# Kernel tuning notes

Measured on AMD Instinct MI355X. Metric: run time of the kernel, lower is better.

Reference implementation:

```python
import jax, jax.numpy as jnp
import numpy as np

B = 32; N = 512; SEQ_LEN = 8
L = 0.05; T_REF = 5.0; V_TH = 20.0; V_RES = 0.0
SQL = float(np.sqrt(L))
BN_EPS = 1e-5

# ---- Dawson-style lookup tables for the LIF moment activation (built once, float64) ----
_XG = np.linspace(-10.0, 4.0, 7001)
_DX = _XG[1] - _XG[0]

def _cumtrapz(y):
    return np.concatenate([[0.0], np.cumsum(0.5 * (y[1:] + y[:-1]) * _DX)])

_phi = np.exp(-_XG ** 2)
_I = np.exp(-100.0) / 20.0 + _cumtrapz(_phi)          # int_{-inf}^x e^{-t^2} dt (asymptotic tail at -10)
_g = np.exp(_XG ** 2) * _I                             # 1st Dawson-like function g(x)
_G = _cumtrapz(_g)                                     # int g dx (rel. to -10)
_h = np.exp(_XG ** 2) * _cumtrapz(_phi * _g ** 2)      # 2nd Dawson-like function h(x)
_H = _cumtrapz(_h)                                     # int h dx

XG = jnp.asarray(_XG, jnp.float32)
GT = jnp.asarray(_g, jnp.float32)
GI = jnp.asarray(_G, jnp.float32)
HI = jnp.asarray(_H, jnp.float32)

def _interp(x, tab):
    return jnp.interp(x, XG, tab)

def moment_activate(u, s, rho):
    # Mnn_Activate_Mean / Std / Corr: LIF moment activation
    s = jnp.maximum(s, 1e-6)
    ub = jnp.clip((V_TH * L - u) / (s * SQL), -10.0, 4.0)
    lb = jnp.clip((V_RES * L - u) / (s * SQL), -10.0, 4.0)
    dG = _interp(ub, GI) - _interp(lb, GI)
    ua = 1.0 / (T_REF + (2.0 / L) * dG)                               # mean firing rate
    dH = jnp.maximum(_interp(ub, HI) - _interp(lb, HI), 0.0)
    sa = jnp.sqrt((8.0 / L ** 2) * dH * ua ** 3)                      # firing std
    dg = _interp(ub, GT) - _interp(lb, GT)
    chi = ua ** 2 * (2.0 / L) * dg / (SQL * jnp.maximum(sa, 1e-9))    # linear response coeff
    eye = jnp.eye(rho.shape[-1], dtype=rho.dtype)
    rho_out = chi[:, :, None] * chi[:, None, :] * rho                 # [B,N,N]
    rho_out = rho_out * (1.0 - eye) + eye                             # unit diagonal
    return ua, sa, rho_out

def linear_corr(W, b, u, s, rho):
    # Mnn_Linear_Corr: mean via affine map, covariance via W C W^T
    u_out = u @ W.T + b
    Cin = rho * s[:, :, None] * s[:, None, :]                         # [B,N,N] covariance
    C = jnp.einsum('bik,lk->bil', jnp.einsum('ij,bjk->bik', W, Cin), W)
    var = jnp.clip(jnp.diagonal(C, axis1=1, axis2=2), 0.0, None)
    s_out = jnp.sqrt(var)
    denom = s_out[:, :, None] * s_out[:, None, :]
    rho_out = jnp.where(denom > 1e-12, C / jnp.maximum(denom, 1e-12), 0.0)
    return u_out, s_out, rho_out

def mexi_hat(n, k=0.3):
    dx = 2.0 * np.pi / n
    x = np.arange(0.0, 2.0 * np.pi, dx)[:n]
    y = np.exp(2.0 * (np.cos(x) - 1.0)) * np.cos(2.0 * x)
    j = np.arange(n)
    idx = (j[None, :] - j[:, None]) % n                               # w[i,:] = y.roll(i)
    return y[idx].astype(np.float32)

def setup_inputs() -> dict:
    ks = jax.random.split(jax.random.key(0), 10)
    u = jax.random.normal(ks[0], (B, N), jnp.float32)
    s = jax.random.uniform(ks[1], (B, N), jnp.float32, 0.1, 1.0)
    A = jax.random.normal(ks[2], (B, N, N), jnp.float32) / np.sqrt(N)
    sym = 0.5 * (A + jnp.swapaxes(A, 1, 2))
    eye = jnp.eye(N, dtype=jnp.float32)
    rho = jnp.clip(sym, -0.5, 0.5) * (1.0 - eye) + eye                # valid-ish corr matrix
    u_ext = jax.random.normal(ks[3], (B, N), jnp.float32)
    s_ext = jax.random.uniform(ks[4], (B, N), jnp.float32, 0.1, 1.0)
    W = 0.02 * jax.random.normal(ks[5], (N, N), jnp.float32) + 0.1 * jnp.asarray(mexi_hat(N))
    b = 0.02 * jax.random.normal(ks[6], (N,), jnp.float32)
    W_ext = 0.02 * jax.random.normal(ks[7], (N, N), jnp.float32)
    b_ext = 0.02 * jax.random.normal(ks[8], (N,), jnp.float32)
    w_mean = 2.5 * jnp.ones((N,), jnp.float32)
    b_mean = 2.5 * jnp.ones((N,), jnp.float32)
    w_mean_ext = 2.5 * jnp.ones((N,), jnp.float32)
    b_mean_ext = 2.5 * jnp.ones((N,), jnp.float32)
    return {'u': u, 's': s, 'rho': rho, 'u_ext': u_ext, 's_ext': s_ext,
            'W': W, 'b': b, 'W_ext': W_ext, 'b_ext': b_ext,
            'w_mean': w_mean, 'b_mean': b_mean,
            'w_mean_ext': w_mean_ext, 'b_mean_ext': b_mean_ext,
            'seq_len': SEQ_LEN}

def reference(u, s, rho, u_ext, s_ext, W, b, W_ext, b_ext,
              w_mean, b_mean, w_mean_ext, b_mean_ext, seq_len):
    # external pathway (Mnn_Linear_without_Corr + BN), computed once
    u_e = u_ext @ W_ext.T + b_ext
    s_e = jnp.sqrt((s_ext ** 2) @ (W_ext ** 2).T)
    mean_e = jnp.mean(u_e, axis=0); var_e = jnp.var(u_e, axis=0)
    f_e = w_mean_ext / jnp.sqrt(var_e + BN_EPS)
    s_e = s_e * jnp.abs(f_e)                                          # Mnn_Std_Bn1d (uses pre-BN stats)
    u_e = (u_e - mean_e) * f_e + b_mean_ext

    def step(carry, _):
        u, s, rho = carry
        u, s, rho = linear_corr(W, b, u, s, rho)
        mean = jnp.mean(u, axis=0); var = jnp.var(u, axis=0)
        f = w_mean / jnp.sqrt(var + BN_EPS)
        s = s * jnp.abs(f)
        u = (u - mean) * f + b_mean
        u = u + u_e
        s = jnp.sqrt(s * s + s_e * s_e)
        return moment_activate(u, s, rho), None

    (u, s, rho), _ = jax.lax.scan(step, (u, s, rho), None, length=seq_len)
    return u, s, rho
```

## Files before the change

### kernel.cpp

```cpp
#include <hip/hip_runtime.h>
#include <math.h>


#define BB 32
#define NN 512
#define SEQ 8
#define TG 7001

typedef float f32x4 __attribute__((ext_vector_type(4)));
typedef short s16x8 __attribute__((ext_vector_type(8)));

#define GL16(g, l) __builtin_amdgcn_global_load_lds( \
    (const __attribute__((address_space(1))) void*)(g), \
    (__attribute__((address_space(3))) void*)(l), 16, 0, 0)

__device__ __forceinline__ unsigned short bf16_rne(float v) {
    unsigned u = __float_as_uint(v);
    u += 0x7FFFu + ((u >> 16) & 1u);
    return (unsigned short)(u >> 16);
}
__device__ __forceinline__ float bf16_f(unsigned short h) {
    return __uint_as_float(((unsigned)h) << 16);
}
__device__ __forceinline__ void split2(float v, unsigned short& h, unsigned short& l) {
    unsigned short hh = bf16_rne(v);
    h = hh;
    l = bf16_rne(v - bf16_f(hh));
}

__device__ __forceinline__ float interp_tab(const float* __restrict__ tab, float x) {
    float t = (x + 10.0f) * 500.0f;
    t = fminf(fmaxf(t, 0.0f), 7000.0f);
    int i0 = (int)t;
    if (i0 > 6999) i0 = 6999;
    float fr = t - (float)i0;
    float a = tab[i0];
    float b = tab[i0 + 1];
    return a + fr * (b - a);
}

__device__ double blk_exscan(double part, double* wsum) {
    int t = threadIdx.x, lane = t & 63, wid = t >> 6;
    double run = part;
    #pragma unroll
    for (int off = 1; off < 64; off <<= 1) {
        double nv = __shfl_up(run, off);
        if (lane >= off) run += nv;
    }
    if (lane == 63) wsum[wid] = run;
    __syncthreads();
    if (t < 16) {
        double v = wsum[t];
        #pragma unroll
        for (int off = 1; off < 16; off <<= 1) {
            double nv = __shfl_up(v, off);
            if (lane >= off) v += nv;
        }
        wsum[t] = v;
    }
    __syncthreads();
    double base = (wid > 0) ? wsum[wid - 1] : 0.0;
    double ex = base + run - part;
    __syncthreads();
    return ex;
}

__global__ __launch_bounds__(1024)
void k_tables(double* __restrict__ expP, double* __restrict__ expM,
              double* __restrict__ gd, double* __restrict__ Ed,
              float* __restrict__ GT, float* __restrict__ GI, float* __restrict__ HI) {
    __shared__ double wsum[16];
    const int t = threadIdx.x;
    const double dx = 14.0 / 7000.0;
    int k0 = t * 7, k1 = k0 + 7;
    if (k1 > TG) k1 = TG;
    if (k0 > TG) k0 = TG;

    for (int k = k0; k < k1; ++k) {
        double x = -10.0 + dx * k;
        expP[k] = exp(x * x);
        expM[k] = exp(-x * x);
    }
    __syncthreads();

    {
        double part = 0.0;
        for (int k = (k0 < 1 ? 1 : k0); k < k1; ++k)
            part += 0.5 * (expM[k - 1] + expM[k]) * dx;
        double run = blk_exscan(part, wsum) + exp(-100.0) / 20.0;
        for (int k = k0; k < k1; ++k) {
            if (k >= 1) run += 0.5 * (expM[k - 1] + expM[k]) * dx;
            double g = expP[k] * run;
            gd[k] = g;
            GT[k] = (float)g;
        }
    }
    __syncthreads();
    {
        double part = 0.0;
        for (int k = (k0 < 1 ? 1 : k0); k < k1; ++k)
            part += 0.5 * (gd[k - 1] + gd[k]) * dx;
        double run = blk_exscan(part, wsum);
        for (int k = k0; k < k1; ++k) {
            if (k >= 1) run += 0.5 * (gd[k - 1] + gd[k]) * dx;
            GI[k] = (float)run;
        }
    }
    __syncthreads();
    {
        double part = 0.0;
        for (int k = (k0 < 1 ? 1 : k0); k < k1; ++k) {
            double ya = expM[k - 1] * gd[k - 1] * gd[k - 1];
            double yb = expM[k] * gd[k] * gd[k];
            part += 0.5 * (ya + yb) * dx;
        }
        double run = blk_exscan(part, wsum);
        for (int k = k0; k < k1; ++k) {
            if (k >= 1) {
                double ya = expM[k - 1] * gd[k - 1] * gd[k - 1];
                double yb = expM[k] * gd[k] * gd[k];
                run += 0.5 * (ya + yb) * dx;
            }
            Ed[k] = run;
        }
    }
    __syncthreads();
    {
        double part = 0.0;
        for (int k = (k0 < 1 ? 1 : k0); k < k1; ++k)
            part += 0.5 * (expP[k - 1] * Ed[k - 1] + expP[k] * Ed[k]) * dx;
        double run = blk_exscan(part, wsum);
        for (int k = k0; k < k1; ++k) {
            if (k >= 1) run += 0.5 * (expP[k - 1] * Ed[k - 1] + expP[k] * Ed[k]) * dx;
            HI[k] = (float)run;
        }
    }
}

__global__ void k_splitW(const float* __restrict__ W,
                         unsigned short* __restrict__ Wh, unsigned short* __restrict__ Wl) {
    int idx = blockIdx.x * 256 + threadIdx.x;
    unsigned short h, l;
    split2(W[idx], h, l);
    Wh[idx] = h; Wl[idx] = l;
}

__global__ void k_splitQ(const float* __restrict__ rho, const float* __restrict__ s,
                         unsigned short* __restrict__ Qh, unsigned short* __restrict__ Ql) {
    size_t idx = (size_t)blockIdx.x * 256 + threadIdx.x;
    int b = (int)(idx >> 18);
    int i = (int)((idx >> 9) & 511);
    int j = (int)(idx & 511);
    float v = rho[idx] * s[b * NN + i] * s[b * NN + j];
    unsigned short h, l;
    split2(v, h, l);
    Qh[idx] = h; Ql[idx] = l;
}

template <int MODE>
__global__ __launch_bounds__(256)
void gemm_mfma(const unsigned short* __restrict__ Ah, const unsigned short* __restrict__ Al,
               long aStride,
               const unsigned short* __restrict__ Bh, const unsigned short* __restrict__ Bl,
               long bStride,
               unsigned short* __restrict__ Oh, unsigned short* __restrict__ Ol,
               float* __restrict__ Of,
               const float* __restrict__ s_lin, const float* __restrict__ chi,
               const float* __restrict__ s_next) {
    __shared__ unsigned short As0[4096], As1[4096], Bs0[4096], Bs1[4096];
    const int b = blockIdx.z;
    const int i0 = blockIdx.y * 128, j0 = blockIdx.x * 128;
    const int tid = threadIdx.x;
    const int w = tid >> 6, lane = tid & 63;
    const int wm = w >> 1, wn = w & 1;

    const unsigned short* Ab_h = Ah + (size_t)b * aStride;
    const unsigned short* Ab_l = Al + (size_t)b * aStride;
    const unsigned short* Bb_h = Bh + (size_t)b * bStride;
    const unsigned short* Bb_l = Bl + (size_t)b * bStride;

    const size_t gA0 = ((size_t)(i0 + (w * 2 + 0) * 16 + (lane >> 2)) << 9) + ((lane & 3) << 3);
    const size_t gA1 = ((size_t)(i0 + (w * 2 + 1) * 16 + (lane >> 2)) << 9) + ((lane & 3) << 3);
    const size_t gB0 = ((size_t)(j0 + (w * 2 + 0) * 16 + (lane >> 2)) << 9) + ((lane & 3) << 3);
    const size_t gB1 = ((size_t)(j0 + (w * 2 + 1) * 16 + (lane >> 2)) << 9) + ((lane & 3) << 3);
    const int lds0 = (w * 2 + 0) * 512;
    const int lds1 = (w * 2 + 1) * 512;

    f32x4 acc[4][4];
    #pragma unroll
    for (int m = 0; m < 4; ++m)
        #pragma unroll
        for (int n = 0; n < 4; ++n) acc[m][n] = (f32x4){0.f, 0.f, 0.f, 0.f};

    const int kg = lane >> 4;
    int aoff[4], boff[4];
    #pragma unroll
    for (int t = 0; t < 4; ++t) {
        aoff[t] = (wm * 64 + t * 16 + (lane & 15)) * 32 + kg * 8;
        boff[t] = (wn * 64 + t * 16 + (lane & 15)) * 32 + kg * 8;
    }

    for (int k0 = 0; k0 < NN; k0 += 32) {
        GL16(Ab_h + gA0 + k0, As0 + lds0);
        GL16(Ab_h + gA1 + k0, As0 + lds1);
        GL16(Ab_l + gA0 + k0, As1 + lds0);
        GL16(Ab_l + gA1 + k0, As1 + lds1);
        GL16(Bb_h + gB0 + k0, Bs0 + lds0);
        GL16(Bb_h + gB1 + k0, Bs0 + lds1);
        GL16(Bb_l + gB0 + k0, Bs1 + lds0);
        GL16(Bb_l + gB1 + k0, Bs1 + lds1);
        __syncthreads();
        s16x8 ah[4], al[4], bh[4], bl[4];
        #pragma unroll
        for (int t = 0; t < 4; ++t) {
            ah[t] = *reinterpret_cast<const s16x8*>(&As0[aoff[t]]);
            al[t] = *reinterpret_cast<const s16x8*>(&As1[aoff[t]]);
            bh[t] = *reinterpret_cast<const s16x8*>(&Bs0[boff[t]]);
            bl[t] = *reinterpret_cast<const s16x8*>(&Bs1[boff[t]]);
        }
        #pragma unroll
        for (int m = 0; m < 4; ++m)
            #pragma unroll
            for (int n = 0; n < 4; ++n) {
                acc[m][n] = __builtin_amdgcn_mfma_f32_16x16x32_bf16(ah[m], bh[n], acc[m][n], 0, 0, 0);
                acc[m][n] = __builtin_amdgcn_mfma_f32_16x16x32_bf16(ah[m], bl[n], acc[m][n], 0, 0, 0);
                acc[m][n] = __builtin_amdgcn_mfma_f32_16x16x32_bf16(al[m], bh[n], acc[m][n], 0, 0, 0);
            }
        __syncthreads();
    }

    const size_t bofs = (size_t)b * NN * NN;
    const int rb = i0 + wm * 64 + (lane >> 4) * 4;
    const int cb = j0 + wn * 64 + (lane & 15);

    if (MODE == 0) {
        #pragma unroll
        for (int m = 0; m < 4; ++m)
            #pragma unroll
            for (int n = 0; n < 4; ++n) {
                int col = cb + n * 16;
                #pragma unroll
                for (int r = 0; r < 4; ++r) {
                    int row = rb + m * 16 + r;
                    size_t idx = bofs + ((size_t)row << 9) + col;
                    unsigned short h, l;
                    split2(acc[m][n][r], h, l);
                    Oh[idx] = h; Ol[idx] = l;
                }
            }
    } else {
        const float* sl = s_lin + b * NN;
        const float* ch = chi + b * NN;
        float sj[4], cj[4], qj[4];
        #pragma unroll
        for (int n = 0; n < 4; ++n) {
            int col = cb + n * 16;
            sj[n] = sl[col];
            cj[n] = ch[col];
            if (MODE == 1) qj[n] = s_next[b * NN + col];
        }
        #pragma unroll
        for (int m = 0; m < 4; ++m)
            #pragma unroll
            for (int r = 0; r < 4; ++r) {
                int row = rb + m * 16 + r;
                float si = sl[row], ci = ch[row];
                float qi = (MODE == 1) ? s_next[b * NN + row] : 0.f;
                #pragma unroll
                for (int n = 0; n < 4; ++n) {
                    int col = cb + n * 16;
                    float denom = si * sj[n];
                    float rv = (denom > 1e-12f) ? (acc[m][n][r] / fmaxf(denom, 1e-12f)) : 0.0f;
                    rv *= ci * cj[n];
                    if (row == col) rv = 1.0f;
                    size_t idx = bofs + ((size_t)row << 9) + col;
                    if (MODE == 1) {
                        unsigned short h, l;
                        split2(rv * qi * qj[n], h, l);
                        Oh[idx] = h; Ol[idx] = l;
                    } else {
                        Of[idx] = rv;
                    }
                }
            }
    }
}

__global__ void k_ext_dots(const float* __restrict__ Wx, const float* __restrict__ bx,
                           const float* __restrict__ ux, const float* __restrict__ sx,
                           float* __restrict__ u_e, float* __restrict__ s_e2) {
    int gw = (blockIdx.x << 2) + (threadIdx.x >> 6);
    int lane = threadIdx.x & 63;
    int b = gw >> 9, i = gw & 511;
    const float* wr = Wx + (size_t)i * NN;
    const float* ub = ux + b * NN;
    const float* sb = sx + b * NN;
    float au = 0.0f, as2 = 0.0f;
    for (int j = lane; j < NN; j += 64) {
        float w = wr[j];
        float s = sb[j];
        au = fmaf(w, ub[j], au);
        as2 = fmaf(w * w, s * s, as2);
    }
    #pragma unroll
    for (int off = 32; off; off >>= 1) {
        au += __shfl_down(au, off);
        as2 += __shfl_down(as2, off);
    }
    if (lane == 0) {
        u_e[b * NN + i] = au + bx[i];
        s_e2[b * NN + i] = as2;
    }
}

__global__ void k_ext_stats(float* __restrict__ u_e, float* __restrict__ s_e2,
                            const float* __restrict__ wmx, const float* __restrict__ bmx) {
    int i = blockIdx.x * blockDim.x + threadIdx.x;
    if (i >= NN) return;
    float m = 0.0f;
    for (int b = 0; b < BB; ++b) m += u_e[b * NN + i];
    m *= (1.0f / BB);
    float v = 0.0f;
    for (int b = 0; b < BB; ++b) {
        float d = u_e[b * NN + i] - m;
        v = fmaf(d, d, v);
    }
    v *= (1.0f / BB);
    float f = wmx[i] / sqrtf(v + 1e-5f);
    float bm = bmx[i];
    for (int b = 0; b < BB; ++b) {
        u_e[b * NN + i] = (u_e[b * NN + i] - m) * f + bm;
        s_e2[b * NN + i] *= f * f;
    }
}

__global__ void k_dots(const float* __restrict__ W, const float* __restrict__ bvec,
                       const float* __restrict__ u,
                       const unsigned short* __restrict__ T1h,
                       const unsigned short* __restrict__ T1l,
                       float* __restrict__ u_lin, float* __restrict__ s_lin) {
    int gw = (blockIdx.x << 2) + (threadIdx.x >> 6);
    int lane = threadIdx.x & 63;
    int b = gw >> 9, i = gw & 511;
    const float* wr = W + (size_t)i * NN;
    const float* ub = u + b * NN;
    const unsigned short* th = T1h + ((size_t)b * NN + i) * NN;
    const unsigned short* tl = T1l + ((size_t)b * NN + i) * NN;
    float au = 0.0f, ad = 0.0f;
    for (int j = lane; j < NN; j += 64) {
        float wv = wr[j];
        au = fmaf(wv, ub[j], au);
        float tv = bf16_f(th[j]) + bf16_f(tl[j]);
        ad = fmaf(wv, tv, ad);
    }
    #pragma unroll
    for (int off = 32; off; off >>= 1) {
        au += __shfl_down(au, off);
        ad += __shfl_down(ad, off);
    }
    if (lane == 0) {
        u_lin[b * NN + i] = au + bvec[i];
        s_lin[b * NN + i] = sqrtf(fmaxf(ad, 0.0f));
    }
}

__global__ void k_stats(const float* __restrict__ u_lin, const float* __restrict__ wm,
                        float* __restrict__ bn_mean, float* __restrict__ bn_f) {
    int i = blockIdx.x * blockDim.x + threadIdx.x;
    if (i >= NN) return;
    float m = 0.0f;
    for (int b = 0; b < BB; ++b) m += u_lin[b * NN + i];
    m *= (1.0f / BB);
    float v = 0.0f;
    for (int b = 0; b < BB; ++b) {
        float d = u_lin[b * NN + i] - m;
        v = fmaf(d, d, v);
    }
    v *= (1.0f / BB);
    bn_mean[i] = m;
    bn_f[i] = wm[i] / sqrtf(v + 1e-5f);
}

__global__ void k_act(const float* __restrict__ u_lin, const float* __restrict__ s_lin,
                      const float* __restrict__ bn_mean, const float* __restrict__ bn_f,
                      const float* __restrict__ b_mean,
                      const float* __restrict__ u_e, const float* __restrict__ s_e2,
                      const float* __restrict__ GT, const float* __restrict__ GI,
                      const float* __restrict__ HI,
                      float* __restrict__ u_out, float* __restrict__ s_out,
                      float* __restrict__ chi) {
    int idx = blockIdx.x * blockDim.x + threadIdx.x;
    int i = idx & 511;
    const float SQL = 0.22360679774997896f;
    float f = bn_f[i];
    float un = (u_lin[idx] - bn_mean[i]) * f + b_mean[i] + u_e[idx];
    float sl = s_lin[idx];
    float sn = sqrtf(sl * sl * f * f + s_e2[idx]);
    float ss = fmaxf(sn, 1e-6f);
    float inv = 1.0f / (ss * SQL);
    float ubx = fminf(fmaxf((1.0f - un) * inv, -10.0f), 4.0f);
    float lbx = fminf(fmaxf((0.0f - un) * inv, -10.0f), 4.0f);
    float dG = interp_tab(GI, ubx) - interp_tab(GI, lbx);
    float ua = 1.0f / (5.0f + 40.0f * dG);
    float dH = fmaxf(interp_tab(HI, ubx) - interp_tab(HI, lbx), 0.0f);
    float sa = sqrtf(3200.0f * dH * ua * ua * ua);
    float dg = interp_tab(GT, ubx) - interp_tab(GT, lbx);
    float ch = ua * ua * 40.0f * dg / (SQL * fmaxf(sa, 1e-9f));
    u_out[idx] = ua;
    s_out[idx] = sa;
    chi[idx] = ch;
}

extern "C" void kernel_launch(void* const* d_in, const int* in_sizes, int n_in,
                              void* d_out, int out_size, void* d_ws, size_t ws_size,
                              hipStream_t stream) {
    (void)in_sizes; (void)n_in; (void)out_size; (void)ws_size;
    const float* u_in       = (const float*)d_in[0];
    const float* s_in       = (const float*)d_in[1];
    const float* rho_in     = (const float*)d_in[2];
    const float* u_ext      = (const float*)d_in[3];
    const float* s_ext      = (const float*)d_in[4];
    const float* W          = (const float*)d_in[5];
    const float* bvec       = (const float*)d_in[6];
    const float* W_ext      = (const float*)d_in[7];
    const float* b_ext      = (const float*)d_in[8];
    const float* w_mean     = (const float*)d_in[9];
    const float* b_mean     = (const float*)d_in[10];
    const float* w_mean_ext = (const float*)d_in[11];
    const float* b_mean_ext = (const float*)d_in[12];

    float* out_u   = (float*)d_out;
    float* out_s   = out_u + BB * NN;
    float* out_rho = out_s + BB * NN;
    unsigned short* Qh = (unsigned short*)out_rho;
    unsigned short* Ql = Qh + (size_t)BB * NN * NN;

    char* base = (char*)d_ws;
    size_t off = 0;
    auto alloc = [&](size_t bytes) -> char* {
        char* p = base + off;
        off += (bytes + 255) & ~(size_t)255;
        return p;
    };
    unsigned short* T1h = (unsigned short*)alloc((size_t)BB * NN * NN * 2);
    unsigned short* T1l = (unsigned short*)alloc((size_t)BB * NN * NN * 2);
    unsigned short* Wh  = (unsigned short*)alloc((size_t)NN * NN * 2);
    unsigned short* Wl  = (unsigned short*)alloc((size_t)NN * NN * 2);
    double* expP = (double*)alloc(TG * 8);
    double* expM = (double*)alloc(TG * 8);
    double* gd   = (double*)alloc(TG * 8);
    double* Ed   = (double*)alloc(TG * 8);
    float* GTt   = (float*)alloc(TG * 4);
    float* GIt   = (float*)alloc(TG * 4);
    float* HIt   = (float*)alloc(TG * 4);
    float* u_e   = (float*)alloc(BB * NN * 4);
    float* s_e2  = (float*)alloc(BB * NN * 4);
    float* uA    = (float*)alloc(BB * NN * 4);
    float* uB2   = (float*)alloc(BB * NN * 4);
    float* sA    = (float*)alloc(BB * NN * 4);
    float* sB2   = (float*)alloc(BB * NN * 4);
    float* u_lin = (float*)alloc(BB * NN * 4);
    float* s_lin = (float*)alloc(BB * NN * 4);
    float* chi_  = (float*)alloc(BB * NN * 4);
    float* bn_m  = (float*)alloc(NN * 4);
    float* bn_f  = (float*)alloc(NN * 4);

    k_tables<<<1, 1024, 0, stream>>>(expP, expM, gd, Ed, GTt, GIt, HIt);
    k_splitW<<<NN * NN / 256, 256, 0, stream>>>(W, Wh, Wl);
    k_splitQ<<<BB * NN * NN / 256, 256, 0, stream>>>(rho_in, s_in, Qh, Ql);
    k_ext_dots<<<BB * NN / 4, 256, 0, stream>>>(W_ext, b_ext, u_ext, s_ext, u_e, s_e2);
    k_ext_stats<<<2, 256, 0, stream>>>(u_e, s_e2, w_mean_ext, b_mean_ext);

    const float* cu = u_in;
    dim3 gg(NN / 128, NN / 128, BB);

    for (int t = 0; t < SEQ; ++t) {
        gemm_mfma<0><<<gg, 256, 0, stream>>>(
            Wh, Wl, 0L, Qh, Ql, (long)NN * NN, T1h, T1l, nullptr, nullptr, nullptr, nullptr);
        k_dots<<<BB * NN / 4, 256, 0, stream>>>(W, bvec, cu, T1h, T1l, u_lin, s_lin);
        k_stats<<<2, 256, 0, stream>>>(u_lin, w_mean, bn_m, bn_f);
        float* nu = (t == SEQ - 1) ? out_u : ((t & 1) ? uA : uB2);
        float* ns = (t == SEQ - 1) ? out_s : ((t & 1) ? sA : sB2);
        k_act<<<BB * NN / 256, 256, 0, stream>>>(
            u_lin, s_lin, bn_m, bn_f, b_mean, u_e, s_e2, GTt, GIt, HIt, nu, ns, chi_);
        if (t < SEQ - 1) {
            gemm_mfma<1><<<gg, 256, 0, stream>>>(
                T1h, T1l, (long)NN * NN, Wh, Wl, 0L, Qh, Ql, nullptr, s_lin, chi_, ns);
        } else {
            gemm_mfma<2><<<gg, 256, 0, stream>>>(
                T1h, T1l, (long)NN * NN, Wh, Wl, 0L, nullptr, nullptr, out_rho, s_lin, chi_, nullptr);
        }
        cu = nu;
    }
}
```

Before: 833.9 us.

## Fuse diagonal variance into GEMM epilogue, swizzle tiles, parallelize table build

The first GEMM epilogue now computes each row's diagonal variance dot product against W and accumulates it with atomics. This removes the pass in k_dots that reread the full T1 intermediate. BN statistics and the activation are merged into one small kernel, and the GEMM grid is flattened with a swizzle that groups tiles sharing operands. The table construction moves exp into a parallel kernel and keeps the scan intermediates in shared memory. The trade-offs are atomics, a 2-block activation kernel that serializes over the batch, and extra W reads in the epilogue.

Result: slower. 924.0 us (+10.8%).

```diff
diff --git a/kernel.cpp b/kernel.cpp
--- a/kernel.cpp
+++ b/kernel.cpp
@@ -39,6 +39,14 @@
     return a + fr * (b - a);
 }
 
+__global__ void k_exp(double* __restrict__ expP, double* __restrict__ expM) {
+    int k = blockIdx.x * 256 + threadIdx.x;
+    if (k >= TG) return;
+    double x = -10.0 + (14.0 / 7000.0) * k;
+    expP[k] = exp(x * x);
+    expM[k] = exp(-x * x);
+}
+
 __device__ double blk_exscan(double part, double* wsum) {
     int t = threadIdx.x, lane = t & 63, wid = t >> 6;
     double run = part;
@@ -66,72 +74,76 @@
 }
 
 __global__ __launch_bounds__(1024)
-void k_tables(double* __restrict__ expP, double* __restrict__ expM,
-              double* __restrict__ gd, double* __restrict__ Ed,
-              float* __restrict__ GT, float* __restrict__ GI, float* __restrict__ HI) {
+void k_scan(const double* __restrict__ expP, const double* __restrict__ expM,
+            float* __restrict__ GT, float* __restrict__ GI, float* __restrict__ HI) {
+    __shared__ double ys[7008];
     __shared__ double wsum[16];
     const int t = threadIdx.x;
     const double dx = 14.0 / 7000.0;
     int k0 = t * 7, k1 = k0 + 7;
     if (k1 > TG) k1 = TG;
     if (k0 > TG) k0 = TG;
-
-    for (int k = k0; k < k1; ++k) {
-        double x = -10.0 + dx * k;
-        expP[k] = exp(x * x);
-        expM[k] = exp(-x * x);
-    }
+    int kls = (k0 < 1) ? 1 : k0;
+
+    for (int k = k0; k < k1; ++k) ys[k] = expM[k];
     __syncthreads();
 
+    double tmp[7];
     {
         double part = 0.0;
-        for (int k = (k0 < 1 ? 1 : k0); k < k1; ++k)
-            part += 0.5 * (expM[k - 1] + expM[k]) * dx;
+        for (int k = kls; k < k1; ++k) part += 0.5 * (ys[k - 1] + ys[k]) * dx;
         double run = blk_exscan(part, wsum) + exp(-100.0) / 20.0;
+        int c = 0;
         for (int k = k0; k < k1; ++k) {
-            if (k >= 1) run += 0.5 * (expM[k - 1] + expM[k]) * dx;
-            double g = expP[k] * run;
-            gd[k] = g;
-            GT[k] = (float)g;
-        }
-    }
-    __syncthreads();
+            if (k >= 1) run += 0.5 * (ys[k - 1] + ys[k]) * dx;
+            tmp[c] = expP[k] * run;
+            GT[k] = (float)tmp[c];
+            ++c;
+        }
+        __syncthreads();
+        c = 0;
+        for (int k = k0; k < k1; ++k) ys[k] = tmp[c++];
+        __syncthreads();
+    }
     {
         double part = 0.0;
-        for (int k = (k0 < 1 ? 1 : k0); k < k1; ++k)
-            part += 0.5 * (gd[k - 1] + gd[k]) * dx;
+        for (int k = kls; k < k1; ++k) part += 0.5 * (ys[k - 1] + ys[k]) * dx;
         double run = blk_exscan(part, wsum);
         for (int k = k0; k < k1; ++k) {
-            if (k >= 1) run += 0.5 * (gd[k - 1] + gd[k]) * dx;
+            if (k >= 1) run += 0.5 * (ys[k - 1] + ys[k]) * dx;
             GI[k] = (float)run;
         }
-    }
-    __syncthreads();
+        __syncthreads();
+    }
     {
         double part = 0.0;
-        for (int k = (k0 < 1 ? 1 : k0); k < k1; ++k) {
-            double ya = expM[k - 1] * gd[k - 1] * gd[k - 1];
-            double yb = expM[k] * gd[k] * gd[k];
+        for (int k = kls; k < k1; ++k) {
+            double ya = expM[k - 1] * ys[k - 1] * ys[k - 1];
+            double yb = expM[k] * ys[k] * ys[k];
             part += 0.5 * (ya + yb) * dx;
         }
+        double run = blk_exscan(part, wsum);
+        int c = 0;
+        for (int k = k0; k < k1; ++k) {
+            if (k >= 1) {
+                double ya = expM[k - 1] * ys[k - 1] * ys[k - 1];
+                double yb = expM[k] * ys[k] * ys[k];
+                run += 0.5 * (ya + yb) * dx;
+            }
+            tmp[c++] = run;
+        }
+        __syncthreads();
+        c = 0;
+        for (int k = k0; k < k1; ++k) ys[k] = tmp[c++];
+        __syncthreads();
+    }
+    {
+        double part = 0.0;
+        for (int k = kls; k < k1; ++k)
+            part += 0.5 * (expP[k - 1] * ys[k - 1] + expP[k] * ys[k]) * dx;
         double run = blk_exscan(part, wsum);
         for (int k = k0; k < k1; ++k) {
-            if (k >= 1) {
-                double ya = expM[k - 1] * gd[k - 1] * gd[k - 1];
-                double yb = expM[k] * gd[k] * gd[k];
-                run += 0.5 * (ya + yb) * dx;
-            }
-            Ed[k] = run;
-        }
-    }
-    __syncthreads();
-    {
-        double part = 0.0;
-        for (int k = (k0 < 1 ? 1 : k0); k < k1; ++k)
-            part += 0.5 * (expP[k - 1] * Ed[k - 1] + expP[k] * Ed[k]) * dx;
-        double run = blk_exscan(part, wsum);
-        for (int k = k0; k < k1; ++k) {
-            if (k >= 1) run += 0.5 * (expP[k - 1] * Ed[k - 1] + expP[k] * Ed[k]) * dx;
+            if (k >= 1) run += 0.5 * (expP[k - 1] * ys[k - 1] + expP[k] * ys[k]) * dx;
             HI[k] = (float)run;
         }
     }
@@ -157,7 +169,7 @@
     Qh[idx] = h; Ql[idx] = l;
 }
 
-template <int MODE>
+template <int MODE, int SWZ>
 __global__ __launch_bounds__(256)
 void gemm_mfma(const unsigned short* __restrict__ Ah, const unsigned short* __restrict__ Al,
                long aStride,
@@ -165,11 +177,18 @@
                long bStride,
                unsigned short* __restrict__ Oh, unsigned short* __restrict__ Ol,
                float* __restrict__ Of,
+               const float* __restrict__ Wf, float* __restrict__ s_var,
                const float* __restrict__ s_lin, const float* __restrict__ chi,
                const float* __restrict__ s_next) {
-    __shared__ unsigned short As0[4096], As1[4096], Bs0[4096], Bs1[4096];
-    const int b = blockIdx.z;
-    const int i0 = blockIdx.y * 128, j0 = blockIdx.x * 128;
+    __shared__ __align__(16) unsigned short As0[4096], As1[4096], Bs0[4096], Bs1[4096];
+    const int id = blockIdx.x;
+    const int member = (id >> 3) & 3;
+    const int g = (id & 7) | ((id >> 5) << 3);
+    const int p = g & 3;
+    const int b = g >> 2;
+    const int xt = (SWZ == 0) ? p : member;
+    const int yt = (SWZ == 0) ? member : p;
+    const int i0 = yt * 128, j0 = xt * 128;
     const int tid = threadIdx.x;
     const int w = tid >> 6, lane = tid & 63;
     const int wm = w >> 1, wn = w & 1;
@@ -234,6 +253,30 @@
     const int cb = j0 + wn * 64 + (lane & 15);
 
     if (MODE == 0) {
+        float dp[16];
+        #pragma unroll
+        for (int m = 0; m < 4; ++m)
+            #pragma unroll
+            for (int r = 0; r < 4; ++r) {
+                int row = rb + m * 16 + r;
+                const float* wrow = Wf + ((size_t)row << 9) + cb;
+                float s = 0.0f;
+                #pragma unroll
+                for (int n = 0; n < 4; ++n) s = fmaf(acc[m][n][r], wrow[n * 16], s);
+                dp[m * 4 + r] = s;
+            }
+        #pragma unroll
+        for (int k = 0; k < 16; ++k) {
+            #pragma unroll
+            for (int off = 1; off < 16; off <<= 1) dp[k] += __shfl_xor(dp[k], off);
+        }
+        if ((lane & 15) == 0) {
+            #pragma unroll
+            for (int k = 0; k < 16; ++k) {
+                int row = rb + (k >> 2) * 16 + (k & 3);
+                atomicAdd(&s_var[b * NN + row], dp[k]);
+            }
+        }
         #pragma unroll
         for (int m = 0; m < 4; ++m)
             #pragma unroll
@@ -334,40 +377,32 @@
     }
 }
 
-__global__ void k_dots(const float* __restrict__ W, const float* __restrict__ bvec,
-                       const float* __restrict__ u,
-                       const unsigned short* __restrict__ T1h,
-                       const unsigned short* __restrict__ T1l,
-                       float* __restrict__ u_lin, float* __restrict__ s_lin) {
+__global__ void k_gemv(const float* __restrict__ W, const float* __restrict__ bvec,
+                       const float* __restrict__ u, float* __restrict__ u_lin) {
     int gw = (blockIdx.x << 2) + (threadIdx.x >> 6);
     int lane = threadIdx.x & 63;
     int b = gw >> 9, i = gw & 511;
     const float* wr = W + (size_t)i * NN;
     const float* ub = u + b * NN;
-    const unsigned short* th = T1h + ((size_t)b * NN + i) * NN;
-    const unsigned short* tl = T1l + ((size_t)b * NN + i) * NN;
-    float au = 0.0f, ad = 0.0f;
-    for (int j = lane; j < NN; j += 64) {
-        float wv = wr[j];
-        au = fmaf(wv, ub[j], au);
-        float tv = bf16_f(th[j]) + bf16_f(tl[j]);
-        ad = fmaf(wv, tv, ad);
-    }
+    float au = 0.0f;
+    for (int j = lane; j < NN; j += 64)
+        au = fmaf(wr[j], ub[j], au);
     #pragma unroll
-    for (int off = 32; off; off >>= 1) {
+    for (int off = 32; off; off >>= 1)
         au += __shfl_down(au, off);
-        ad += __shfl_down(ad, off);
-    }
-    if (lane == 0) {
+    if (lane == 0)
         u_lin[b * NN + i] = au + bvec[i];
-        s_lin[b * NN + i] = sqrtf(fmaxf(ad, 0.0f));
-    }
-}
-
-__global__ void k_stats(const float* __restrict__ u_lin, const float* __restrict__ wm,
-                        float* __restrict__ bn_mean, float* __restrict__ bn_f) {
-    int i = blockIdx.x * blockDim.x + threadIdx.x;
-    if (i >= NN) return;
+}
+
+__global__ void k_bnact(const float* __restrict__ u_lin, float* __restrict__ s_var,
+                        const float* __restrict__ wm, const float* __restrict__ bmv,
+                        const float* __restrict__ u_e, const float* __restrict__ s_e2,
+                        const float* __restrict__ GT, const float* __restrict__ GI,
+                        const float* __restrict__ HI,
+                        float* __restrict__ u_out, float* __restrict__ s_out,
+                        float* __restrict__ chi, float* __restrict__ s_lin) {
+    int i = blockIdx.x * 256 + threadIdx.x;
+    const float SQL = 0.22360679774997896f;
     float m = 0.0f;
     for (int b = 0; b < BB; ++b) m += u_lin[b * NN + i];
     m *= (1.0f / BB);
@@ -377,38 +412,30 @@
         v = fmaf(d, d, v);
     }
     v *= (1.0f / BB);
-    bn_mean[i] = m;
-    bn_f[i] = wm[i] / sqrtf(v + 1e-5f);
-}
-
-__global__ void k_act(const float* __restrict__ u_lin, const float* __restrict__ s_lin,
-                      const float* __restrict__ bn_mean, const float* __restrict__ bn_f,
-                      const float* __restrict__ b_mean,
-                      const float* __restrict__ u_e, const float* __restrict__ s_e2,
-                      const float* __restrict__ GT, const float* __restrict__ GI,
-                      const float* __restrict__ HI,
-                      float* __restrict__ u_out, float* __restrict__ s_out,
-                      float* __restrict__ chi) {
-    int idx = blockIdx.x * blockDim.x + threadIdx.x;
-    int i = idx & 511;
-    const float SQL = 0.22360679774997896f;
-    float f = bn_f[i];
-    float un = (u_lin[idx] - bn_mean[i]) * f + b_mean[i] + u_e[idx];
-    float sl = s_lin[idx];
-    float sn = sqrtf(sl * sl * f * f + s_e2[idx]);
-    float ss = fmaxf(sn, 1e-6f);
-    float inv = 1.0f / (ss * SQL);
-    float ubx = fminf(fmaxf((1.0f - un) * inv, -10.0f), 4.0f);
-    float lbx = fminf(fmaxf((0.0f - un) * inv, -10.0f), 4.0f);
-    float dG = interp_tab(GI, ubx) - interp_tab(GI, lbx);
-    float ua = 1.0f / (5.0f + 40.0f * dG);
-    float dH = fmaxf(interp_tab(HI, ubx) - interp_tab(HI, lbx), 0.0f);
-    float sa = sqrtf(3200.0f * dH * ua * ua * ua);
-    float dg = interp_tab(GT, ubx) - interp_tab(GT, lbx);
-    float ch = ua * ua * 40.0f * dg / (SQL * fmaxf(sa, 1e-9f));
-    u_out[idx] = ua;
-    s_out[idx] = sa;
-    chi[idx] = ch;
+    float f = wm[i] / sqrtf(v + 1e-5f);
+    float bm = bmv[i];
+    for (int b = 0; b < BB; ++b) {
+        int idx = b * NN + i;
+        float sv = s_var[idx];
+        s_var[idx] = 0.0f;
+        float s_l = sqrtf(fmaxf(sv, 0.0f));
+        s_lin[idx] = s_l;
+        float un = (u_lin[idx] - m) * f + bm + u_e[idx];
+        float sn = sqrtf(s_l * s_l * f * f + s_e2[idx]);
+        float ss = fmaxf(sn, 1e-6f);
+        float inv = 1.0f / (ss * SQL);
+        float ubx = fminf(fmaxf((1.0f - un) * inv, -10.0f), 4.0f);
+        float lbx = fminf(fmaxf((0.0f - un) * inv, -10.0f), 4.0f);
+        float dG = interp_tab(GI, ubx) - interp_tab(GI, lbx);
+        float ua = 1.0f / (5.0f + 40.0f * dG);
+        float dH = fmaxf(interp_tab(HI, ubx) - interp_tab(HI, lbx), 0.0f);
+        float sa = sqrtf(3200.0f * dH * ua * ua * ua);
+        float dg = interp_tab(GT, ubx) - interp_tab(GT, lbx);
+        float ch = ua * ua * 40.0f * dg / (SQL * fmaxf(sa, 1e-9f));
+        u_out[idx] = ua;
+        s_out[idx] = sa;
+        chi[idx] = ch;
+    }
 }
 
 extern "C" void kernel_launch(void* const* d_in, const int* in_sizes, int n_in,
@@ -448,8 +475,6 @@
     unsigned short* Wl  = (unsigned short*)alloc((size_t)NN * NN * 2);
     double* expP = (double*)alloc(TG * 8);
     double* expM = (double*)alloc(TG * 8);
-    double* gd   = (double*)alloc(TG * 8);
-    double* Ed   = (double*)alloc(TG * 8);
     float* GTt   = (float*)alloc(TG * 4);
     float* GIt   = (float*)alloc(TG * 4);
     float* HIt   = (float*)alloc(TG * 4);
@@ -462,33 +487,35 @@
     float* u_lin = (float*)alloc(BB * NN * 4);
     float* s_lin = (float*)alloc(BB * NN * 4);
     float* chi_  = (float*)alloc(BB * NN * 4);
-    float* bn_m  = (float*)alloc(NN * 4);
-    float* bn_f  = (float*)alloc(NN * 4);
-
-    k_tables<<<1, 1024, 0, stream>>>(expP, expM, gd, Ed, GTt, GIt, HIt);
+    float* s_var = (float*)alloc(BB * NN * 4);
+
+    k_exp<<<28, 256, 0, stream>>>(expP, expM);
+    k_scan<<<1, 1024, 0, stream>>>(expP, expM, GTt, GIt, HIt);
     k_splitW<<<NN * NN / 256, 256, 0, stream>>>(W, Wh, Wl);
     k_splitQ<<<BB * NN * NN / 256, 256, 0, stream>>>(rho_in, s_in, Qh, Ql);
     k_ext_dots<<<BB * NN / 4, 256, 0, stream>>>(W_ext, b_ext, u_ext, s_ext, u_e, s_e2);
     k_ext_stats<<<2, 256, 0, stream>>>(u_e, s_e2, w_mean_ext, b_mean_ext);
+    hipMemsetAsync(s_var, 0, BB * NN * 4, stream);
 
     const float* cu = u_in;
-    dim3 gg(NN / 128, NN / 128, BB);
 
     for (int t = 0; t < SEQ; ++t) {
-        gemm_mfma<0><<<gg, 256, 0, stream>>>(
-            Wh, Wl, 0L, Qh, Ql, (long)NN * NN, T1h, T1l, nullptr, nullptr, nullptr, nullptr);
-        k_dots<<<BB * NN / 4, 256, 0, stream>>>(W, bvec, cu, T1h, T1l, u_lin, s_lin);
-        k_stats<<<2, 256, 0, stream>>>(u_lin, w_mean, bn_m, bn_f);
+        gemm_mfma<0, 0><<<512, 256, 0, stream>>>(
+            Wh, Wl, 0L, Qh, Ql, (long)NN * NN, T1h, T1l, nullptr,
+            W, s_var, nullptr, nullptr, nullptr);
+        k_gemv<<<BB * NN / 4, 256, 0, stream>>>(W, bvec, cu, u_lin);
         float* nu = (t == SEQ - 1) ? out_u : ((t & 1) ? uA : uB2);
         float* ns = (t == SEQ - 1) ? out_s : ((t & 1) ? sA : sB2);
-        k_act<<<BB * NN / 256, 256, 0, stream>>>(
-            u_lin, s_lin, bn_m, bn_f, b_mean, u_e, s_e2, GTt, GIt, HIt, nu, ns, chi_);
+        k_bnact<<<2, 256, 0, stream>>>(
+            u_lin, s_var, w_mean, b_mean, u_e, s_e2, GTt, GIt, HIt, nu, ns, chi_, s_lin);
         if (t < SEQ - 1) {
-            gemm_mfma<1><<<gg, 256, 0, stream>>>(
-                T1h, T1l, (long)NN * NN, Wh, Wl, 0L, Qh, Ql, nullptr, s_lin, chi_, ns);
+            gemm_mfma<1, 1><<<512, 256, 0, stream>>>(
+                T1h, T1l, (long)NN * NN, Wh, Wl, 0L, Qh, Ql, nullptr,
+                nullptr, nullptr, s_lin, chi_, ns);
         } else {
-            gemm_mfma<2><<<gg, 256, 0, stream>>>(
-                T1h, T1l, (long)NN * NN, Wh, Wl, 0L, nullptr, nullptr, out_rho, s_lin, chi_, nullptr);
+            gemm_mfma<2, 1><<<512, 256, 0, stream>>>(
+                T1h, T1l, (long)NN * NN, Wh, Wl, 0L, nullptr, nullptr, out_rho,
+                nullptr, nullptr, s_lin, chi_, nullptr);
         }
         cu = nu;
     }
```
